# Kernel optimization log

Measured on AMD Instinct MI355X. Metric: run time of the kernel, lower is better.

Reference implementation:

```python
import jax, jax.numpy as jnp
import numpy as np

B, H_IMG, W_IMG, C_IMG, NP = 8, 384, 384, 3, 6
DELTA = 10
TOL = 1e-3
LAM = 0.05          # lambda_ (Charbonnier scale)
MAX_ITER = 12
RIDGE = 1e-6


def _cubic(s):
    # Keys bicubic convolution kernel, a = -0.5
    a = -0.5
    s = jnp.abs(s)
    s2 = s * s
    s3 = s2 * s
    w1 = (a + 2.0) * s3 - (a + 3.0) * s2 + 1.0
    w2 = a * s3 - 5.0 * a * s2 + 8.0 * a * s - 4.0 * a
    return jnp.where(s <= 1.0, w1, jnp.where(s < 2.0, w2, 0.0))


def _bicubic(I, xg, yg):
    # I: [b,H,W,C]; xg,yg: [b,H,W] sample coordinates
    Bn, Hh, Ww, C = I.shape
    x0 = jnp.floor(xg)
    y0 = jnp.floor(yg)
    tx = xg - x0
    ty = yg - y0
    xi = x0.astype(jnp.int32)
    yi = y0.astype(jnp.int32)
    bidx = jnp.arange(Bn)[:, None, None]
    out = jnp.zeros(I.shape, I.dtype)
    for j in range(4):           # fixed 4x4 tap stencil
        wy = _cubic(ty - (j - 1))
        yy = jnp.clip(yi + (j - 1), 0, Hh - 1)
        for k in range(4):
            wx = _cubic(tx - (k - 1))
            xx = jnp.clip(xi + (k - 1), 0, Ww - 1)
            out = out + (wy * wx)[..., None] * I[bidx, yy, xx, :]
    return out


def _params2matrix(p):
    # AFFINITY: x' = x + p0 + p2*x + p3*y ; y' = y + p1 + p4*x + p5*y
    zero = jnp.zeros_like(p[:, 0])
    one = jnp.ones_like(p[:, 0])
    r0 = jnp.stack([1.0 + p[:, 2], p[:, 3], p[:, 0]], -1)
    r1 = jnp.stack([p[:, 4], 1.0 + p[:, 5], p[:, 1]], -1)
    r2 = jnp.stack([zero, zero, one], -1)
    return jnp.stack([r0, r1, r2], 1)


def _matrix2params(M):
    M = M / M[:, 2:3, 2:3]
    return jnp.stack([M[:, 0, 2], M[:, 1, 2], M[:, 0, 0] - 1.0,
                      M[:, 0, 1], M[:, 1, 0], M[:, 1, 1] - 1.0], -1)


def _gradients(I):
    # central differences, zero-padded at the borders (as in compute_gradients)
    Ix = jnp.pad((I[:, :, 2:, :] - I[:, :, :-2, :]) * 0.5,
                 ((0, 0), (0, 0), (1, 1), (0, 0)))
    Iy = jnp.pad((I[:, 2:, :, :] - I[:, :-2, :, :]) * 0.5,
                 ((0, 0), (1, 1), (0, 0), (0, 0)))
    return Ix, Iy


def setup_inputs() -> dict:
    key = jax.random.key(0)
    k1, k2 = jax.random.split(key)
    I1 = jax.random.uniform(k1, (B, H_IMG, W_IMG, C_IMG), jnp.float32)
    I2 = jax.random.uniform(k2, (B, H_IMG, W_IMG, C_IMG), jnp.float32)
    p = jnp.zeros((B, NP), jnp.float32)
    return {"I1": I1, "I2": I2, "p": p}


def _forward(I1, I2, p):
    Bn, Hh, Ww, C = I1.shape
    x = jnp.arange(Ww, dtype=jnp.float32)
    y = jnp.arange(Hh, dtype=jnp.float32)
    X, Y = jnp.meshgrid(x, y)
    ones = jnp.ones_like(X)
    zeros = jnp.zeros_like(X)
    # AFFINITY Jacobian, split into Jx / Jy halves: [H,W,6]
    Jx = jnp.stack([ones, zeros, X, Y, zeros, zeros], -1)
    Jy = jnp.stack([zeros, ones, zeros, zeros, X, Y], -1)
    Ix, Iy = _gradients(I1)
    # steepest-descent images: [b,H,W,C,6]
    DIJ = Ix[..., None] * Jx[None, :, :, None, :] + Iy[..., None] * Jy[None, :, :, None, :]
    rows_ok = (jnp.arange(Hh) >= DELTA) & (jnp.arange(Hh) < Hh - DELTA)
    cols_ok = (jnp.arange(Ww) >= DELTA) & (jnp.arange(Ww) < Ww - DELTA)
    valid1 = (rows_ok[:, None] & cols_ok[None, :])[None, :, :, None]  # [1,H,W,1]
    coords = jnp.stack([X, Y, ones], 0)  # [3,H,W]
    eye = jnp.eye(NP, dtype=jnp.float32)

    def warp(pcur):
        M = _params2matrix(pcur)
        g = jnp.einsum('bij,jhw->bihw', M, coords)
        xg, yg = g[:, 0], g[:, 1]
        Iw = _bicubic(I2, xg, yg)
        gx = jnp.round(xg).astype(jnp.int32)
        gy = jnp.round(yg).astype(jnp.int32)
        wmask = ((gx >= DELTA) & (gx <= Ww - DELTA) &
                 (gy >= DELTA) & (gy <= Hh - DELTA))[..., None]
        return Iw, wmask

    def step(carry, _):
        pcur, done = carry
        Iw, wmask = carry_warp = warp(pcur)
        m = wmask & valid1
        DI = jnp.where(m, Iw - I1, 0.0)
        # Charbonnier influence weight psi(e) = 1/sqrt(1 + (e/lam)^2)
        w = jnp.where(m, jax.lax.rsqrt(1.0 + (DI / LAM) ** 2), 0.0)
        bvec = jnp.einsum('bhwcm,bhwc->bm', DIJ, w * DI)
        Hm = jnp.einsum('bhwcm,bhwcn->bmn', DIJ * w[..., None], DIJ)
        dp = jnp.linalg.solve(Hm + RIDGE * eye, bvec[..., None])[..., 0]
        # inverse-compositional update: W(p) <- W(p) o W(dp)^-1
        Mn = _params2matrix(pcur) @ jnp.linalg.inv(_params2matrix(dp))
        p_new = _matrix2params(Mn)
        conv = jnp.linalg.norm(dp, axis=-1) < TOL
        p_out = jnp.where(done[:, None], pcur, p_new)
        return (p_out, done | conv), None

    (pf, _), _ = jax.lax.scan(step, (p, jnp.zeros((Bn,), bool)), None, length=MAX_ITER)
    Iw, wmask = warp(pf)
    m = wmask & valid1
    DI = jnp.where(m, Iw - I1, 0.0)
    rho = 2.0 * LAM * LAM * (jnp.sqrt(1.0 + (DI / LAM) ** 2) - 1.0)
    mb = jnp.broadcast_to(m, DI.shape)
    cnt = jnp.sum(mb.astype(jnp.float32), axis=(1, 2, 3))
    err = jnp.sum(jnp.where(mb, rho, 0.0), axis=(1, 2, 3)) / jnp.maximum(cnt, 1.0)
    return pf, err, DI, Iw


def reference(I1, I2, p):
    return _forward(I1, I2, p)
```

## Files before the change

kernel.cpp:

```cpp
#include <hip/hip_runtime.h>
#include <math.h>

#define BB 8
#define HH 384
#define WW 384
#define NPAR 6
#define DEL 10
#define MAXIT 12
#define NACC 24
#define HWPIX (HH*WW)
#define NRT4 91
#define NR2 8
#define W_STG 76
#define PITCH2 77
#define NWIN 6
#define NR2F 6
#define PITCHF 141
#define WSF 140
#define KB_ 8
#define SPS 32

typedef float vf4 __attribute__((ext_vector_type(4)));
typedef vf4 uvf4 __attribute__((aligned(4)));
typedef float f2v __attribute__((ext_vector_type(2), aligned(4)));
typedef float lf4 __attribute__((ext_vector_type(4)));

__device__ __forceinline__ vf4 ldv4(const float* p) { return *(const uvf4*)p; }

__device__ __forceinline__ lf4 ldpx3(const float* __restrict__ Ib, int pixoff) {
    const int fo = pixoff * 3;
    if (fo + 4 <= HWPIX * 3) {
        vf4 v = ldv4(Ib + fo);
        return (lf4){v.x, v.y, v.z, 0.f};
    }
    vf4 v = ldv4(Ib + fo - 1);
    return (lf4){v.y, v.z, v.w, 0.f};
}

__device__ __forceinline__ float cubicw(float s) {
    s = fabsf(s);
    float s2 = s * s, s3 = s2 * s;
    float w1 = 1.5f * s3 - 2.5f * s2 + 1.0f;
    float w2 = -0.5f * s3 + 2.5f * s2 - 4.0f * s + 2.0f;
    return (s <= 1.0f) ? w1 : ((s < 2.0f) ? w2 : 0.0f);
}

__device__ __forceinline__ void bicubic3_fast(const float* __restrict__ Ib, double xg, double yg, float Iw[3]) {
    double fx = floor(xg), fy = floor(yg);
    float tx = (float)(xg - fx), ty = (float)(yg - fy);
    int xi = (int)fx, yi = (int)fy;
    float wx[4], wyv[4];
#pragma unroll
    for (int k = 0; k < 4; k++) { wx[k] = cubicw(tx - (float)(k - 1)); wyv[k] = cubicw(ty - (float)(k - 1)); }
    Iw[0] = 0.f; Iw[1] = 0.f; Iw[2] = 0.f;
    const float* base = Ib + (yi - 1) * (WW * 3) + (xi - 1) * 3;
#pragma unroll
    for (int j = 0; j < 4; j++) {
        const float* r = base + j * (WW * 3);
        vf4 v0 = ldv4(r), v1 = ldv4(r + 4), v2 = ldv4(r + 8);
        float r0 = fmaf(wx[0], v0.x, 0.f); r0 = fmaf(wx[1], v0.w, r0); r0 = fmaf(wx[2], v1.z, r0); r0 = fmaf(wx[3], v2.y, r0);
        float r1 = fmaf(wx[0], v0.y, 0.f); r1 = fmaf(wx[1], v1.x, r1); r1 = fmaf(wx[2], v1.w, r1); r1 = fmaf(wx[3], v2.z, r1);
        float r2 = fmaf(wx[0], v0.z, 0.f); r2 = fmaf(wx[1], v1.y, r2); r2 = fmaf(wx[2], v2.x, r2); r2 = fmaf(wx[3], v2.w, r2);
        Iw[0] = fmaf(wyv[j], r0, Iw[0]);
        Iw[1] = fmaf(wyv[j], r1, Iw[1]);
        Iw[2] = fmaf(wyv[j], r2, Iw[2]);
    }
}

__device__ __forceinline__ void bicubic3_gen(const float* __restrict__ Ib, double xg, double yg, float Iw[3]) {
    double fx = floor(xg), fy = floor(yg);
    int xi = (int)fx, yi = (int)fy;
    float tx = (float)(xg - fx), ty = (float)(yg - fy);
    float wx[4], wyv[4];
    int xx[4], yy[4];
#pragma unroll
    for (int k = 0; k < 4; k++) {
        wx[k] = cubicw(tx - (float)(k - 1)); wyv[k] = cubicw(ty - (float)(k - 1));
        xx[k] = min(max(xi + k - 1, 0), WW - 1);
        yy[k] = min(max(yi + k - 1, 0), HH - 1);
    }
    Iw[0] = 0.f; Iw[1] = 0.f; Iw[2] = 0.f;
#pragma unroll
    for (int j = 0; j < 4; j++) {
        const float* row = Ib + yy[j] * (WW * 3);
        float r0 = 0.f, r1 = 0.f, r2 = 0.f;
#pragma unroll
        for (int k = 0; k < 4; k++) {
            const float* q = row + xx[k] * 3;
            r0 = fmaf(wx[k], q[0], r0); r1 = fmaf(wx[k], q[1], r1); r2 = fmaf(wx[k], q[2], r2);
        }
        Iw[0] = fmaf(wyv[j], r0, Iw[0]);
        Iw[1] = fmaf(wyv[j], r1, Iw[1]);
        Iw[2] = fmaf(wyv[j], r2, Iw[2]);
    }
}

template<int P>
__device__ __forceinline__ void bicubic3_lds(const lf4* __restrict__ T, int ssx, int ssy,
                                             float tx, float ty, float Iw[3]) {
    float wx[4], wyv[4];
#pragma unroll
    for (int k = 0; k < 4; k++) { wx[k] = cubicw(tx - (float)(k - 1)); wyv[k] = cubicw(ty - (float)(k - 1)); }
    Iw[0] = 0.f; Iw[1] = 0.f; Iw[2] = 0.f;
    const lf4* bp = T + (ssy - 1) * P + (ssx - 1);
#pragma unroll
    for (int j = 0; j < 4; j++) {
        lf4 t0 = bp[j * P + 0], t1 = bp[j * P + 1], t2 = bp[j * P + 2], t3 = bp[j * P + 3];
        float r0 = fmaf(wx[0], t0.x, 0.f); r0 = fmaf(wx[1], t1.x, r0); r0 = fmaf(wx[2], t2.x, r0); r0 = fmaf(wx[3], t3.x, r0);
        float r1 = fmaf(wx[0], t0.y, 0.f); r1 = fmaf(wx[1], t1.y, r1); r1 = fmaf(wx[2], t2.y, r1); r1 = fmaf(wx[3], t3.y, r1);
        float r2 = fmaf(wx[0], t0.z, 0.f); r2 = fmaf(wx[1], t1.z, r2); r2 = fmaf(wx[2], t2.z, r2); r2 = fmaf(wx[3], t3.z, r2);
        Iw[0] = fmaf(wyv[j], r0, Iw[0]);
        Iw[1] = fmaf(wyv[j], r1, Iw[1]);
        Iw[2] = fmaf(wyv[j], r2, Iw[2]);
    }
}

__device__ __forceinline__
void solve6_fast(const double* __restrict__ Sb, const double* __restrict__ pc,
                 double pn[6], int* convp) {
    const double b0 = Sb[0], b1 = Sb[3], b2 = Sb[1], b3 = Sb[2], b4 = Sb[4], b5 = Sb[5];
    const double h00 = Sb[6]  + 1e-6, h01 = Sb[12], h02 = Sb[7],  h03 = Sb[8],  h04 = Sb[13], h05 = Sb[14];
    const double h11 = Sb[18] + 1e-6, h12 = Sb[13], h13 = Sb[14], h14 = Sb[19], h15 = Sb[20];
    const double h22 = Sb[9]  + 1e-6, h23 = Sb[10], h24 = Sb[15], h25 = Sb[16];
    const double h33 = Sb[11] + 1e-6, h34 = Sb[16], h35 = Sb[17];
    const double h44 = Sb[21] + 1e-6, h45 = Sb[22];
    const double h55 = Sb[23] + 1e-6;

    const double l00 = sqrt(h00);
    const double i0 = 1.0 / l00;
    const double l10 = h01 * i0, l20 = h02 * i0, l30 = h03 * i0, l40 = h04 * i0, l50 = h05 * i0;
    const double l11 = sqrt(h11 - l10 * l10);
    const double i1 = 1.0 / l11;
    const double l21 = (h12 - l20 * l10) * i1;
    const double l31 = (h13 - l30 * l10) * i1;
    const double l41 = (h14 - l40 * l10) * i1;
    const double l51 = (h15 - l50 * l10) * i1;
    const double l22 = sqrt(h22 - l20 * l20 - l21 * l21);
    const double i2 = 1.0 / l22;
    const double l32 = (h23 - l30 * l20 - l31 * l21) * i2;
    const double l42 = (h24 - l40 * l20 - l41 * l21) * i2;
    const double l52 = (h25 - l50 * l20 - l51 * l21) * i2;
    const double l33 = sqrt(h33 - l30 * l30 - l31 * l31 - l32 * l32);
    const double i3 = 1.0 / l33;
    const double l43 = (h34 - l40 * l30 - l41 * l31 - l42 * l32) * i3;
    const double l53 = (h35 - l50 * l30 - l51 * l31 - l52 * l32) * i3;
    const double l44 = sqrt(h44 - l40 * l40 - l41 * l41 - l42 * l42 - l43 * l43);
    const double i4 = 1.0 / l44;
    const double l54 = (h45 - l50 * l40 - l51 * l41 - l52 * l42 - l53 * l43) * i4;
    const double l55 = sqrt(h55 - l50 * l50 - l51 * l51 - l52 * l52 - l53 * l53 - l54 * l54);
    const double i5 = 1.0 / l55;

    const double y0 = b0 * i0;
    const double y1 = (b1 - l10 * y0) * i1;
    const double y2 = (b2 - l20 * y0 - l21 * y1) * i2;
    const double y3 = (b3 - l30 * y0 - l31 * y1 - l32 * y2) * i3;
    const double y4 = (b4 - l40 * y0 - l41 * y1 - l42 * y2 - l43 * y3) * i4;
    const double y5 = (b5 - l50 * y0 - l51 * y1 - l52 * y2 - l53 * y3 - l54 * y4) * i5;

    const double d5 = y5 * i5;
    const double d4 = (y4 - l54 * d5) * i4;
    const double d3 = (y3 - l43 * d4 - l53 * d5) * i3;
    const double d2 = (y2 - l32 * d3 - l42 * d4 - l52 * d5) * i2;
    const double d1 = (y1 - l21 * d2 - l31 * d3 - l41 * d4 - l51 * d5) * i1;
    const double d0 = (y0 - l10 * d1 - l20 * d2 - l30 * d3 - l40 * d4 - l50 * d5) * i0;

    const double nrm = sqrt(d0*d0 + d1*d1 + d2*d2 + d3*d3 + d4*d4 + d5*d5);
    *convp = (nrm < 1e-3) ? 1 : 0;

    const double m00 = 1.0 + pc[2], m01 = pc[3], m02 = pc[0];
    const double m10 = pc[4], m11 = 1.0 + pc[5], m12 = pc[1];
    const double q00 = 1.0 + d2, q01 = d3, q02 = d0;
    const double q10 = d4, q11 = 1.0 + d5, q12 = d1;
    const double det = q00 * q11 - q01 * q10;
    const double j00 = q11 / det, j01 = -q01 / det;
    const double j10 = -q10 / det, j11 = q00 / det;
    const double jt0 = -(j00 * q02 + j01 * q12);
    const double jt1 = -(j10 * q02 + j11 * q12);
    const double n00 = m00 * j00 + m01 * j10;
    const double n01 = m00 * j01 + m01 * j11;
    const double n02 = m00 * jt0 + m01 * jt1 + m02;
    const double n10 = m10 * j00 + m11 * j10;
    const double n11 = m10 * j01 + m11 * j11;
    const double n12 = m10 * jt0 + m11 * jt1 + m12;
    pn[0] = n02;
    pn[1] = n12;
    pn[2] = n00 - 1.0;
    pn[3] = n01;
    pn[4] = n10;
    pn[5] = n11 - 1.0;
}

extern "C" __global__ __launch_bounds__(256)
void k_init(const float* __restrict__ p0, double* __restrict__ p_store,
            int* __restrict__ done0, double* __restrict__ S_part_all,
            double* __restrict__ Sf_part) {
    const int idx = blockIdx.x * 256 + threadIdx.x;
    const int n = MAXIT * KB_ * BB * SPS;
    for (int i = idx; i < n; i += gridDim.x * 256) S_part_all[i] = 0.0;
    if (blockIdx.x == 0) {
        const int tid = threadIdx.x;
        if (tid < KB_ * BB * 4) Sf_part[tid] = 0.0;
        if (tid < BB * NPAR) p_store[tid] = (double)p0[tid];
        if (tid < BB) done0[tid] = 0;
    }
}

extern "C" __global__ __launch_bounds__(256, 8)
void k_iter(const float* __restrict__ I1, const float* __restrict__ I2,
            const double* __restrict__ p_in, const int* __restrict__ done_in,
            const double* __restrict__ S_in, double* __restrict__ S_out,
            double* __restrict__ p_out_g, int* __restrict__ done_out_g,
            int first) {
    __shared__ __align__(16) double SMEMD[1664];
    __shared__ double Ssum[NACC];
    __shared__ double pbc[NPAR];
    __shared__ int dbc;
    lf4* SMEM = (lf4*)SMEMD;
    const int tid = threadIdx.x;
    const int b = blockIdx.y;
    const int tix = blockIdx.x;
    const int rt = tix / NWIN, win = tix - rt * NWIN;
    const int y0 = 10 + rt * 4;
    const int x0 = 10 + win * 64;
    const int sx0 = x0 - 6;

    double pp[NPAR];
#pragma unroll
    for (int i = 0; i < NPAR; i++) pp[i] = p_in[b * NPAR + i];
    {
        const double pM10 = pp[4], pM11 = 1.0 + pp[5], pM12 = pp[1];
        const double ygc = pM10 * (double)(x0 + 32) + pM11 * ((double)y0 + 1.5) + pM12;
        const int r0 = (int)fmin(fmax(floor(ygc) - 3.0, -100000.0), 100000.0);
        const float* I2b = I2 + (size_t)b * HWPIX * 3;
        for (int i = tid; i < NR2 * W_STG; i += 256) {
            const int r = i / W_STG, c = i - r * W_STG;
            const int gr = min(max(r0 + r, 0), HH - 1);
            const int gc = min(sx0 + c, WW - 1);
            SMEM[r * PITCH2 + c] = ldpx3(I2b, gr * WW + gc);
        }
    }
    const double pM10_ = pp[4], pM11_ = 1.0 + pp[5], pM12_ = pp[1];
    const double ygc_ = pM10_ * (double)(x0 + 32) + pM11_ * ((double)y0 + 1.5) + pM12_;
    const int r0 = (int)fmin(fmax(floor(ygc_) - 3.0, -100000.0), 100000.0);

    if (!first && tid < NACC) {
        double a0 = 0.0, a1 = 0.0;
#pragma unroll
        for (int k = 0; k < KB_; k += 2) {
            a0 += S_in[((size_t)(k * BB + b)) * SPS + tid];
            a1 += S_in[((size_t)((k + 1) * BB + b)) * SPS + tid];
        }
        Ssum[tid] = a0 + a1;
    }
    __syncthreads();

    if (tid == 0) {
        if (first) {
#pragma unroll
            for (int i = 0; i < NPAR; i++) pbc[i] = pp[i];
            dbc = done_in[b];
        } else {
            if (done_in[b]) {
#pragma unroll
                for (int i = 0; i < NPAR; i++) pbc[i] = pp[i];
                dbc = 1;
            } else {
                double pn[6]; int conv;
                solve6_fast(Ssum, p_in + b * NPAR, pn, &conv);
#pragma unroll
                for (int i = 0; i < NPAR; i++) pbc[i] = pn[i];
                dbc = conv;
            }
            if (blockIdx.x == 0) {
#pragma unroll
                for (int i = 0; i < NPAR; i++) p_out_g[b * NPAR + i] = pbc[i];
                done_out_g[b] = dbc;
            }
        }
    }
    __syncthreads();
    if (dbc) return;

    const double M00 = 1.0 + pbc[2], M01 = pbc[3], M02 = pbc[0];
    const double M10 = pbc[4], M11 = 1.0 + pbc[5], M12 = pbc[1];
    const float* I1b = I1 + (size_t)b * HWPIX * 3;
    const float* I2b = I2 + (size_t)b * HWPIX * 3;

    const int wid = tid >> 6, lane = tid & 63;
    const int y = y0 + wid;
    const double Y = (double)y;
    const double Bx = M01 * Y + M02;
    const double By = M11 * Y + M12;

    const int x = x0 + lane;
    const double X = (double)x;
    const double xg = fma(M00, X, Bx);
    const double yg = fma(M10, X, By);
    const double gx = rint(xg), gy = rint(yg);
    const bool ok = (x < WW - DEL) &&
                    (gx >= (double)DEL && gx <= (double)(WW - DEL) &&
                     gy >= (double)DEL && gy <= (double)(HH - DEL));
    const double fx = floor(xg), fy = floor(yg);
    const int xi = (int)fx, yi = (int)fy;
    const float tx = (float)(xg - fx), ty = (float)(yg - fy);
    const int sxi = xi - sx0, syi = yi - r0;
    const bool inwin = ok && (sxi >= 1) && (sxi <= W_STG - 3) && (syi >= 1) && (syi <= NR2 - 3);

    float Iw[3];
    if (ok && !inwin) {
        bicubic3_fast(I2b, xg, yg, Iw);
    } else {
        const int ssx = inwin ? sxi : 8;
        const int ssy = inwin ? syi : 2;
        bicubic3_lds<PITCH2>(SMEM, ssx, ssy, tx, ty, Iw);
    }

    const int xc = min(x, WW - DEL - 1);
    const int pixL = y * WW + xc;
    const float* c = I1b + pixL * 3;
    vf4 u0 = ldv4(c - 3);
    vf4 u1 = ldv4(c + 1);
    float cr2 = c[5];
    vf4 uu = ldv4(c - WW * 3);
    vf4 ud = ldv4(c + WW * 3);

    const float cl[3] = {u0.x, u0.y, u0.z};
    const float cv[3] = {u0.w, u1.x, u1.y};
    const float cr[3] = {u1.z, u1.w, cr2};
    const float cu[3] = {uu.x, uu.y, uu.z};
    const float cd[3] = {ud.x, ud.y, ud.z};

    const float msk = ok ? 1.0f : 0.0f;
    float Af = 0.f, Bf = 0.f, Cf = 0.f, T0f = 0.f, T1f = 0.f;
#pragma unroll
    for (int ch = 0; ch < 3; ch++) {
        const float Ix = (cr[ch] - cl[ch]) * 0.5f;
        const float Iy = (cd[ch] - cu[ch]) * 0.5f;
        const float d = Iw[ch] - cv[ch];
        const float u = d * 20.0f;
        const float w = msk / sqrtf(fmaf(u, u, 1.0f));
        const float wd = w * d;
        T0f = fmaf(Ix, wd, T0f);
        T1f = fmaf(Iy, wd, T1f);
        const float wIx = w * Ix;
        Af = fmaf(wIx, Ix, Af);
        Bf = fmaf(wIx, Iy, Bf);
        Cf = fmaf(w * Iy, Iy, Cf);
    }
    const double T0 = (double)T0f, T1 = (double)T1f;
    const double A = (double)Af, Bd = (double)Bf, Cd = (double)Cf;
    const double XX = X * X;
    double s[13];
    s[0] = T0;  s[1] = T0 * X;
    s[2] = T1;  s[3] = T1 * X;
    s[4] = A;   s[5] = A * X;   s[6] = A * XX;
    s[7] = Bd;  s[8] = Bd * X;  s[9] = Bd * XX;
    s[10] = Cd; s[11] = Cd * X; s[12] = Cd * XX;

#pragma unroll
    for (int i = 0; i < 13; i++) s[i] += __shfl_down(s[i], 32, 64);

    __syncthreads();
    double* scr = SMEMD;
    if (lane < 32) {
        double* o = scr + ((size_t)(wid * 32 + lane)) * 13;
#pragma unroll
        for (int i = 0; i < 13; i++) o[i] = s[i];
    }
    __syncthreads();

    if (tid < NACC) {
        const unsigned long long CLO = 0x9787456454232010ULL;
        const unsigned long long CHI = 0x00000000abcaba78ULL;
        const unsigned long long YPW = 0x0000910910910410ULL;
        const int cix = (int)(((tid < 16) ? (CLO >> (tid * 4)) : (CHI >> ((tid - 16) * 4))) & 0xF);
        const int pw  = (int)((YPW >> (tid * 2)) & 0x3);
        double acc = 0.0;
        for (int w = 0; w < 4; w++) {
            const double* basep = scr + ((size_t)(w * 32)) * 13 + cix;
            double part = 0.0;
            for (int l = 0; l < 32; l++) part += basep[(size_t)l * 13];
            const double Yw = (double)(y0 + w);
            const double f = (pw == 0) ? 1.0 : ((pw == 1) ? Yw : Yw * Yw);
            acc = fma(f, part, acc);
        }
        const int bkt = blockIdx.x & (KB_ - 1);
        unsafeAtomicAdd(&S_out[((size_t)(bkt * BB + b)) * SPS + tid], acc);
    }
}

extern "C" __global__ __launch_bounds__(256, 8)
void k_final_map(const float* __restrict__ I1, const float* __restrict__ I2,
                 const double* __restrict__ p_in, const int* __restrict__ done_in,
                 const double* __restrict__ S_in, double* __restrict__ pf_g,
                 float* __restrict__ DI_out, float* __restrict__ Iw_out,
                 double* __restrict__ Sf_part) {
    __shared__ lf4 I2S[NR2F * PITCHF];
    __shared__ double wsum[4][2];
    __shared__ double Ssum[NACC];
    __shared__ double pbc[NPAR];
    const int tid = threadIdx.x;
    const int b = blockIdx.y;
    const int tix = blockIdx.x;
    const int rt = tix / 3, win = tix - rt * 3;
    const int y0 = rt * 2;
    const int x0 = win * 128;
    const int sx0 = x0 - 6;

    double pp[NPAR];
#pragma unroll
    for (int i = 0; i < NPAR; i++) pp[i] = p_in[b * NPAR + i];
    const double pM10 = pp[4], pM11 = 1.0 + pp[5], pM12 = pp[1];
    const double ygc = pM10 * (double)(x0 + 64) + pM11 * ((double)y0 + 0.5) + pM12;
    const int r0 = (int)fmin(fmax(floor(ygc) - 2.0, -100000.0), 100000.0);
    {
        const float* I2b = I2 + (size_t)b * HWPIX * 3;
        for (int i = tid; i < NR2F * WSF; i += 256) {
            const int r = i / WSF, c = i - r * WSF;
            const int gr = min(max(r0 + r, 0), HH - 1);
            const int gc = min(max(sx0 + c, 0), WW - 1);
            I2S[r * PITCHF + c] = ldpx3(I2b, gr * WW + gc);
        }
    }
    if (tid < NACC) {
        double a0 = 0.0, a1 = 0.0;
#pragma unroll
        for (int k = 0; k < KB_; k += 2) {
            a0 += S_in[((size_t)(k * BB + b)) * SPS + tid];
            a1 += S_in[((size_t)((k + 1) * BB + b)) * SPS + tid];
        }
        Ssum[tid] = a0 + a1;
    }
    __syncthreads();
    if (tid == 0) {
        if (done_in[b]) {
#pragma unroll
            for (int i = 0; i < NPAR; i++) pbc[i] = pp[i];
        } else {
            double pn[6]; int conv;
            solve6_fast(Ssum, p_in + b * NPAR, pn, &conv);
#pragma unroll
            for (int i = 0; i < NPAR; i++) pbc[i] = pn[i];
        }
        if (blockIdx.x == 0) {
#pragma unroll
            for (int i = 0; i < NPAR; i++) pf_g[b * NPAR + i] = pbc[i];
        }
    }
    __syncthreads();

    const double M00 = 1.0 + pbc[2], M01 = pbc[3], M02 = pbc[0];
    const double M10 = pbc[4], M11 = 1.0 + pbc[5], M12 = pbc[1];
    const float* I1b = I1 + (size_t)b * HWPIX * 3;
    const float* I2b = I2 + (size_t)b * HWPIX * 3;
    float* DIb = DI_out + (size_t)b * HWPIX * 3;
    float* Iwb = Iw_out + (size_t)b * HWPIX * 3;

    const int row = tid >> 7;
    const int x = x0 + (tid & 127);
    const int y = y0 + row;
    const int pix = y * WW + x;

    const double X = (double)x, Yd = (double)y;
    const double xg = fma(M00, X, fma(M01, Yd, M02));
    const double yg = fma(M10, X, fma(M11, Yd, M12));
    const double fx = floor(xg), fy = floor(yg);
    const int xi = (int)fx, yi = (int)fy;
    const float tx = (float)(xg - fx), ty = (float)(yg - fy);
    const int sxi = xi - sx0, syi = yi - r0;
    const bool inwin = (sxi >= 1) && (sxi <= WSF - 3) && (syi >= 1) && (syi <= NR2F - 3);

    float Iwp[3];
    if (inwin) bicubic3_lds<PITCHF>(I2S, sxi, syi, tx, ty, Iwp);
    else       bicubic3_gen(I2b, xg, yg, Iwp);

    const bool v1 = (x >= DEL) && (x < WW - DEL) && (y >= DEL) && (y < HH - DEL);
    const double gx = rint(xg), gy = rint(yg);
    const bool wm = (gx >= (double)DEL && gx <= (double)(WW - DEL) &&
                     gy >= (double)DEL && gy <= (double)(HH - DEL));
    const bool mp = v1 && wm;

    const float* cbase = I1b + (size_t)pix * 3;
    const float cv0 = cbase[0], cv1 = cbase[1], cv2 = cbase[2];

    {
        float* wp = Iwb + (size_t)pix * 3;
        *(f2v*)wp = (f2v){Iwp[0], Iwp[1]};
        wp[2] = Iwp[2];
    }
    double rho_s = 0.0, cnt_s = 0.0;
    {
        const float cvv[3] = {cv0, cv1, cv2};
        float dv[3];
#pragma unroll
        for (int ch = 0; ch < 3; ch++) {
            const float d1 = mp ? (Iwp[ch] - cvv[ch]) : 0.0f;
            dv[ch] = d1;
            if (mp) {
                const float u = d1 * 20.0f;
                rho_s += (double)(0.005f * (sqrtf(fmaf(u, u, 1.0f)) - 1.0f));
            }
        }
        if (mp) cnt_s += 3.0;
        float* dp_ = DIb + (size_t)pix * 3;
        *(f2v*)dp_ = (f2v){dv[0], dv[1]};
        dp_[2] = dv[2];
    }

#pragma unroll
    for (int off = 32; off >= 1; off >>= 1) {
        rho_s += __shfl_down(rho_s, off, 64);
        cnt_s += __shfl_down(cnt_s, off, 64);
    }
    const int wv = tid >> 6, lane = tid & 63;
    if (lane == 0) { wsum[wv][0] = rho_s; wsum[wv][1] = cnt_s; }
    __syncthreads();
    if (tid < 2) {
        double sv = wsum[0][tid] + wsum[1][tid] + wsum[2][tid] + wsum[3][tid];
        const int bkt = blockIdx.x & (KB_ - 1);
        unsafeAtomicAdd(&Sf_part[((size_t)(bkt * BB + b)) * 4 + tid], sv);
    }
}

extern "C" __global__ void k_finish(const double* __restrict__ p_fin,
                                    const double* __restrict__ Sf_part,
                                    float* __restrict__ out) {
    const int tid = threadIdx.x;
    if (tid < BB * NPAR) out[tid] = (float)p_fin[tid];
    if (tid >= 48 && tid < 48 + BB) {
        const int b = tid - 48;
        double rs = 0.0, cs = 0.0;
#pragma unroll
        for (int k = 0; k < KB_; k++) {
            rs += Sf_part[((size_t)(k * BB + b)) * 4 + 0];
            cs += Sf_part[((size_t)(k * BB + b)) * 4 + 1];
        }
        out[48 + b] = (float)(rs / fmax(cs, 1.0));
    }
}

extern "C" void kernel_launch(void* const* d_in, const int* in_sizes, int n_in,
                              void* d_out, int out_size, void* d_ws, size_t ws_size,
                              hipStream_t stream) {
    const float* I1 = (const float*)d_in[0];
    const float* I2 = (const float*)d_in[1];
    const float* p0 = (const float*)d_in[2];
    float* out = (float*)d_out;

    double* p_store = (double*)d_ws;
    int* done_flags = (int*)((char*)d_ws + 4992);
    double* S_part_all = (double*)((char*)d_ws + 5408);
    double* Sf_part = (double*)((char*)d_ws + 202016);

    k_init<<<32, 256, 0, stream>>>(p0, p_store, done_flags, S_part_all, Sf_part);

    const size_t SIT = (size_t)KB_ * BB * SPS;
    dim3 gridI(NRT4 * NWIN, BB), blkI(256);
    for (int it = 0; it < MAXIT; it++) {
        const int first = (it == 0) ? 1 : 0;
        const double* p_in = p_store + (size_t)(first ? 0 : (it - 1)) * BB * NPAR;
        const int* d_in_f = done_flags + (first ? 0 : (it - 1)) * BB;
        const double* S_in = S_part_all + (size_t)(first ? 0 : (it - 1)) * SIT;
        k_iter<<<gridI, blkI, 0, stream>>>(I1, I2, p_in, d_in_f, S_in,
                                           S_part_all + (size_t)it * SIT,
                                           p_store + (size_t)it * BB * NPAR,
                                           done_flags + it * BB, first);
    }
    float* DI_out = out + 56;
    float* Iw_out = out + 56 + (size_t)BB * HWPIX * 3;
    dim3 gridF(192 * 3, BB), blkF(256);
    k_final_map<<<gridF, blkF, 0, stream>>>(I1, I2,
                                            p_store + (size_t)11 * BB * NPAR,
                                            done_flags + 11 * BB,
                                            S_part_all + (size_t)11 * SIT,
                                            p_store + (size_t)MAXIT * BB * NPAR,
                                            DI_out, Iw_out, Sf_part);
    k_finish<<<1, 64, 0, stream>>>(p_store + (size_t)MAXIT * BB * NPAR, Sf_part, out);
}
```

Before: 450.2 us.

## Solve 6x6 system once in last-block epilogue instead of per block

Each iteration kernel now uses a two-level atomic counter to detect the last finishing block. Only that block reduces the partial sums and solves the 6x6 system for all batches, writing the next parameters and done flags. Before, every block of the following launch re-read the partials and ran solve6 redundantly in a single thread before starting work. This takes the serial solve off the critical path of all blocks, at the cost of atomic counters, acquire-release ordering and a tail epilogue in one block. It also depends on the release/acquire semantics making the atomically added partials visible to that last block.

```diff
diff --git a/kernel.cpp b/kernel.cpp
--- a/kernel.cpp
+++ b/kernel.cpp
@@ -14,6 +14,9 @@
 #define W_STG 76
 #define PITCH2 77
 #define NWIN 6
+#define NBX (NRT4*NWIN)
+#define L1N 91
+#define L1CNT (6*BB)
 #define NR2F 6
 #define PITCHF 141
 #define WSF 140
@@ -193,10 +196,11 @@
 extern "C" __global__ __launch_bounds__(256)
 void k_init(const float* __restrict__ p0, double* __restrict__ p_store,
             int* __restrict__ done0, double* __restrict__ S_part_all,
-            double* __restrict__ Sf_part) {
+            double* __restrict__ Sf_part, unsigned int* __restrict__ cnt) {
     const int idx = blockIdx.x * 256 + threadIdx.x;
     const int n = MAXIT * KB_ * BB * SPS;
     for (int i = idx; i < n; i += gridDim.x * 256) S_part_all[i] = 0.0;
+    for (int i = idx; i < MAXIT * (L1N + 1); i += gridDim.x * 256) cnt[i] = 0u;
     if (blockIdx.x == 0) {
         const int tid = threadIdx.x;
         if (tid < KB_ * BB * 4) Sf_part[tid] = 0.0;
@@ -208,197 +212,194 @@
 extern "C" __global__ __launch_bounds__(256, 8)
 void k_iter(const float* __restrict__ I1, const float* __restrict__ I2,
             const double* __restrict__ p_in, const int* __restrict__ done_in,
-            const double* __restrict__ S_in, double* __restrict__ S_out,
-            double* __restrict__ p_out_g, int* __restrict__ done_out_g,
-            int first) {
+            double* __restrict__ S_out, double* __restrict__ p_out,
+            int* __restrict__ done_out, unsigned int* __restrict__ c1,
+            unsigned int* __restrict__ c2) {
     __shared__ __align__(16) double SMEMD[1664];
-    __shared__ double Ssum[NACC];
-    __shared__ double pbc[NPAR];
-    __shared__ int dbc;
+    __shared__ int lastflag;
     lf4* SMEM = (lf4*)SMEMD;
+    double* scr = SMEMD;
     const int tid = threadIdx.x;
     const int b = blockIdx.y;
     const int tix = blockIdx.x;
-    const int rt = tix / NWIN, win = tix - rt * NWIN;
-    const int y0 = 10 + rt * 4;
-    const int x0 = 10 + win * 64;
-    const int sx0 = x0 - 6;
-
-    double pp[NPAR];
-#pragma unroll
-    for (int i = 0; i < NPAR; i++) pp[i] = p_in[b * NPAR + i];
-    {
-        const double pM10 = pp[4], pM11 = 1.0 + pp[5], pM12 = pp[1];
-        const double ygc = pM10 * (double)(x0 + 32) + pM11 * ((double)y0 + 1.5) + pM12;
+    const int dn = done_in[b];
+
+    if (!dn) {
+        const int rt = tix / NWIN, win = tix - rt * NWIN;
+        const int y0 = 10 + rt * 4;
+        const int x0 = 10 + win * 64;
+        const int sx0 = x0 - 6;
+
+        double pp[NPAR];
+#pragma unroll
+        for (int i = 0; i < NPAR; i++) pp[i] = p_in[b * NPAR + i];
+        const double M00 = 1.0 + pp[2], M01 = pp[3], M02 = pp[0];
+        const double M10 = pp[4], M11 = 1.0 + pp[5], M12 = pp[1];
+        const float* I1b = I1 + (size_t)b * HWPIX * 3;
+        const float* I2b = I2 + (size_t)b * HWPIX * 3;
+
+        const double ygc = M10 * (double)(x0 + 32) + M11 * ((double)y0 + 1.5) + M12;
         const int r0 = (int)fmin(fmax(floor(ygc) - 3.0, -100000.0), 100000.0);
-        const float* I2b = I2 + (size_t)b * HWPIX * 3;
         for (int i = tid; i < NR2 * W_STG; i += 256) {
             const int r = i / W_STG, c = i - r * W_STG;
             const int gr = min(max(r0 + r, 0), HH - 1);
             const int gc = min(sx0 + c, WW - 1);
             SMEM[r * PITCH2 + c] = ldpx3(I2b, gr * WW + gc);
         }
-    }
-    const double pM10_ = pp[4], pM11_ = 1.0 + pp[5], pM12_ = pp[1];
-    const double ygc_ = pM10_ * (double)(x0 + 32) + pM11_ * ((double)y0 + 1.5) + pM12_;
-    const int r0 = (int)fmin(fmax(floor(ygc_) - 3.0, -100000.0), 100000.0);
-
-    if (!first && tid < NACC) {
-        double a0 = 0.0, a1 = 0.0;
-#pragma unroll
-        for (int k = 0; k < KB_; k += 2) {
-            a0 += S_in[((size_t)(k * BB + b)) * SPS + tid];
-            a1 += S_in[((size_t)((k + 1) * BB + b)) * SPS + tid];
-        }
-        Ssum[tid] = a0 + a1;
-    }
+        __syncthreads();
+
+        const int wid = tid >> 6, lane = tid & 63;
+        const int y = y0 + wid;
+        const double Y = (double)y;
+        const double Bx = M01 * Y + M02;
+        const double By = M11 * Y + M12;
+        const int x = x0 + lane;
+        const double X = (double)x;
+        const double xg = fma(M00, X, Bx);
+        const double yg = fma(M10, X, By);
+        const double gx = rint(xg), gy = rint(yg);
+        const bool ok = (x < WW - DEL) &&
+                        (gx >= (double)DEL && gx <= (double)(WW - DEL) &&
+                         gy >= (double)DEL && gy <= (double)(HH - DEL));
+        const double fx = floor(xg), fy = floor(yg);
+        const int xi = (int)fx, yi = (int)fy;
+        const float tx = (float)(xg - fx), ty = (float)(yg - fy);
+        const int sxi = xi - sx0, syi = yi - r0;
+        const bool inwin = ok && (sxi >= 1) && (sxi <= W_STG - 3) && (syi >= 1) && (syi <= NR2 - 3);
+
+        float Iw[3];
+        if (ok && !inwin) {
+            bicubic3_fast(I2b, xg, yg, Iw);
+        } else {
+            const int ssx = inwin ? sxi : 8;
+            const int ssy = inwin ? syi : 2;
+            bicubic3_lds<PITCH2>(SMEM, ssx, ssy, tx, ty, Iw);
+        }
+
+        const int xc = min(x, WW - DEL - 1);
+        const int pixL = y * WW + xc;
+        const float* c = I1b + pixL * 3;
+        vf4 u0 = ldv4(c - 3);
+        vf4 u1 = ldv4(c + 1);
+        float cr2 = c[5];
+        vf4 uu = ldv4(c - WW * 3);
+        vf4 ud = ldv4(c + WW * 3);
+
+        const float cl[3] = {u0.x, u0.y, u0.z};
+        const float cv[3] = {u0.w, u1.x, u1.y};
+        const float cr[3] = {u1.z, u1.w, cr2};
+        const float cu[3] = {uu.x, uu.y, uu.z};
+        const float cd[3] = {ud.x, ud.y, ud.z};
+
+        const float msk = ok ? 1.0f : 0.0f;
+        float Af = 0.f, Bf = 0.f, Cf = 0.f, T0f = 0.f, T1f = 0.f;
+#pragma unroll
+        for (int ch = 0; ch < 3; ch++) {
+            const float Ix = (cr[ch] - cl[ch]) * 0.5f;
+            const float Iy = (cd[ch] - cu[ch]) * 0.5f;
+            const float d = Iw[ch] - cv[ch];
+            const float u = d * 20.0f;
+            const float w = msk / sqrtf(fmaf(u, u, 1.0f));
+            const float wd = w * d;
+            T0f = fmaf(Ix, wd, T0f);
+            T1f = fmaf(Iy, wd, T1f);
+            const float wIx = w * Ix;
+            Af = fmaf(wIx, Ix, Af);
+            Bf = fmaf(wIx, Iy, Bf);
+            Cf = fmaf(w * Iy, Iy, Cf);
+        }
+        const double T0 = (double)T0f, T1 = (double)T1f;
+        const double A = (double)Af, Bd = (double)Bf, Cd = (double)Cf;
+        const double XX = X * X;
+        double s[13];
+        s[0] = T0;  s[1] = T0 * X;
+        s[2] = T1;  s[3] = T1 * X;
+        s[4] = A;   s[5] = A * X;   s[6] = A * XX;
+        s[7] = Bd;  s[8] = Bd * X;  s[9] = Bd * XX;
+        s[10] = Cd; s[11] = Cd * X; s[12] = Cd * XX;
+
+#pragma unroll
+        for (int i = 0; i < 13; i++) s[i] += __shfl_down(s[i], 32, 64);
+
+        __syncthreads();
+        if (lane < 32) {
+            double* o = scr + ((size_t)(wid * 32 + lane)) * 13;
+#pragma unroll
+            for (int i = 0; i < 13; i++) o[i] = s[i];
+        }
+        __syncthreads();
+
+        if (tid < NACC) {
+            const unsigned long long CLO = 0x9787456454232010ULL;
+            const unsigned long long CHI = 0x00000000abcaba78ULL;
+            const unsigned long long YPW = 0x0000910910910410ULL;
+            const int cix = (int)(((tid < 16) ? (CLO >> (tid * 4)) : (CHI >> ((tid - 16) * 4))) & 0xF);
+            const int pw  = (int)((YPW >> (tid * 2)) & 0x3);
+            double acc = 0.0;
+            for (int w = 0; w < 4; w++) {
+                const double* basep = scr + ((size_t)(w * 32)) * 13 + cix;
+                double part = 0.0;
+                for (int l = 0; l < 32; l++) part += basep[(size_t)l * 13];
+                const double Yw = (double)(y0 + w);
+                const double f = (pw == 0) ? 1.0 : ((pw == 1) ? Yw : Yw * Yw);
+                acc = fma(f, part, acc);
+            }
+            const int bkt = tix & (KB_ - 1);
+            unsafeAtomicAdd(&S_out[((size_t)(bkt * BB + b)) * SPS + tid], acc);
+        }
+    }
+
     __syncthreads();
-
     if (tid == 0) {
-        if (first) {
-#pragma unroll
-            for (int i = 0; i < NPAR; i++) pbc[i] = pp[i];
-            dbc = done_in[b];
-        } else {
-            if (done_in[b]) {
-#pragma unroll
-                for (int i = 0; i < NPAR; i++) pbc[i] = pp[i];
-                dbc = 1;
+        lastflag = 0;
+        const unsigned o1 = __hip_atomic_fetch_add(&c1[tix % L1N], 1u,
+                                __ATOMIC_ACQ_REL, __HIP_MEMORY_SCOPE_AGENT);
+        if (o1 == (unsigned)(L1CNT - 1)) {
+            const unsigned o2 = __hip_atomic_fetch_add(c2, 1u,
+                                    __ATOMIC_ACQ_REL, __HIP_MEMORY_SCOPE_AGENT);
+            if (o2 == (unsigned)(L1N - 1)) lastflag = 1;
+        }
+    }
+    __syncthreads();
+    if (lastflag) {
+        double* FSUM = SMEMD;
+        if (tid < BB * NACC) {
+            const int bt = tid / NACC, a = tid - bt * NACC;
+            double sv = 0.0;
+#pragma unroll
+            for (int k = 0; k < KB_; k++)
+                sv += __hip_atomic_load(&S_out[((size_t)(k * BB + bt)) * SPS + a],
+                                        __ATOMIC_RELAXED, __HIP_MEMORY_SCOPE_AGENT);
+            FSUM[bt * NACC + a] = sv;
+        }
+        __syncthreads();
+        if (tid < BB) {
+            const int bt = tid;
+            double pc[NPAR], pn[NPAR];
+#pragma unroll
+            for (int i = 0; i < NPAR; i++) pc[i] = p_in[bt * NPAR + i];
+            if (done_in[bt]) {
+#pragma unroll
+                for (int i = 0; i < NPAR; i++) p_out[bt * NPAR + i] = pc[i];
+                done_out[bt] = 1;
             } else {
-                double pn[6]; int conv;
-                solve6_fast(Ssum, p_in + b * NPAR, pn, &conv);
-#pragma unroll
-                for (int i = 0; i < NPAR; i++) pbc[i] = pn[i];
-                dbc = conv;
+                int conv;
+                solve6_fast(&FSUM[bt * NACC], pc, pn, &conv);
+#pragma unroll
+                for (int i = 0; i < NPAR; i++) p_out[bt * NPAR + i] = pn[i];
+                done_out[bt] = conv;
             }
-            if (blockIdx.x == 0) {
-#pragma unroll
-                for (int i = 0; i < NPAR; i++) p_out_g[b * NPAR + i] = pbc[i];
-                done_out_g[b] = dbc;
-            }
-        }
-    }
-    __syncthreads();
-    if (dbc) return;
-
-    const double M00 = 1.0 + pbc[2], M01 = pbc[3], M02 = pbc[0];
-    const double M10 = pbc[4], M11 = 1.0 + pbc[5], M12 = pbc[1];
-    const float* I1b = I1 + (size_t)b * HWPIX * 3;
-    const float* I2b = I2 + (size_t)b * HWPIX * 3;
-
-    const int wid = tid >> 6, lane = tid & 63;
-    const int y = y0 + wid;
-    const double Y = (double)y;
-    const double Bx = M01 * Y + M02;
-    const double By = M11 * Y + M12;
-
-    const int x = x0 + lane;
-    const double X = (double)x;
-    const double xg = fma(M00, X, Bx);
-    const double yg = fma(M10, X, By);
-    const double gx = rint(xg), gy = rint(yg);
-    const bool ok = (x < WW - DEL) &&
-                    (gx >= (double)DEL && gx <= (double)(WW - DEL) &&
-                     gy >= (double)DEL && gy <= (double)(HH - DEL));
-    const double fx = floor(xg), fy = floor(yg);
-    const int xi = (int)fx, yi = (int)fy;
-    const float tx = (float)(xg - fx), ty = (float)(yg - fy);
-    const int sxi = xi - sx0, syi = yi - r0;
-    const bool inwin = ok && (sxi >= 1) && (sxi <= W_STG - 3) && (syi >= 1) && (syi <= NR2 - 3);
-
-    float Iw[3];
-    if (ok && !inwin) {
-        bicubic3_fast(I2b, xg, yg, Iw);
-    } else {
-        const int ssx = inwin ? sxi : 8;
-        const int ssy = inwin ? syi : 2;
-        bicubic3_lds<PITCH2>(SMEM, ssx, ssy, tx, ty, Iw);
-    }
-
-    const int xc = min(x, WW - DEL - 1);
-    const int pixL = y * WW + xc;
-    const float* c = I1b + pixL * 3;
-    vf4 u0 = ldv4(c - 3);
-    vf4 u1 = ldv4(c + 1);
-    float cr2 = c[5];
-    vf4 uu = ldv4(c - WW * 3);
-    vf4 ud = ldv4(c + WW * 3);
-
-    const float cl[3] = {u0.x, u0.y, u0.z};
-    const float cv[3] = {u0.w, u1.x, u1.y};
-    const float cr[3] = {u1.z, u1.w, cr2};
-    const float cu[3] = {uu.x, uu.y, uu.z};
-    const float cd[3] = {ud.x, ud.y, ud.z};
-
-    const float msk = ok ? 1.0f : 0.0f;
-    float Af = 0.f, Bf = 0.f, Cf = 0.f, T0f = 0.f, T1f = 0.f;
-#pragma unroll
-    for (int ch = 0; ch < 3; ch++) {
-        const float Ix = (cr[ch] - cl[ch]) * 0.5f;
-        const float Iy = (cd[ch] - cu[ch]) * 0.5f;
-        const float d = Iw[ch] - cv[ch];
-        const float u = d * 20.0f;
-        const float w = msk / sqrtf(fmaf(u, u, 1.0f));
-        const float wd = w * d;
-        T0f = fmaf(Ix, wd, T0f);
-        T1f = fmaf(Iy, wd, T1f);
-        const float wIx = w * Ix;
-        Af = fmaf(wIx, Ix, Af);
-        Bf = fmaf(wIx, Iy, Bf);
-        Cf = fmaf(w * Iy, Iy, Cf);
-    }
-    const double T0 = (double)T0f, T1 = (double)T1f;
-    const double A = (double)Af, Bd = (double)Bf, Cd = (double)Cf;
-    const double XX = X * X;
-    double s[13];
-    s[0] = T0;  s[1] = T0 * X;
-    s[2] = T1;  s[3] = T1 * X;
-    s[4] = A;   s[5] = A * X;   s[6] = A * XX;
-    s[7] = Bd;  s[8] = Bd * X;  s[9] = Bd * XX;
-    s[10] = Cd; s[11] = Cd * X; s[12] = Cd * XX;
-
-#pragma unroll
-    for (int i = 0; i < 13; i++) s[i] += __shfl_down(s[i], 32, 64);
-
-    __syncthreads();
-    double* scr = SMEMD;
-    if (lane < 32) {
-        double* o = scr + ((size_t)(wid * 32 + lane)) * 13;
-#pragma unroll
-        for (int i = 0; i < 13; i++) o[i] = s[i];
-    }
-    __syncthreads();
-
-    if (tid < NACC) {
-        const unsigned long long CLO = 0x9787456454232010ULL;
-        const unsigned long long CHI = 0x00000000abcaba78ULL;
-        const unsigned long long YPW = 0x0000910910910410ULL;
-        const int cix = (int)(((tid < 16) ? (CLO >> (tid * 4)) : (CHI >> ((tid - 16) * 4))) & 0xF);
-        const int pw  = (int)((YPW >> (tid * 2)) & 0x3);
-        double acc = 0.0;
-        for (int w = 0; w < 4; w++) {
-            const double* basep = scr + ((size_t)(w * 32)) * 13 + cix;
-            double part = 0.0;
-            for (int l = 0; l < 32; l++) part += basep[(size_t)l * 13];
-            const double Yw = (double)(y0 + w);
-            const double f = (pw == 0) ? 1.0 : ((pw == 1) ? Yw : Yw * Yw);
-            acc = fma(f, part, acc);
-        }
-        const int bkt = blockIdx.x & (KB_ - 1);
-        unsafeAtomicAdd(&S_out[((size_t)(bkt * BB + b)) * SPS + tid], acc);
+        }
     }
 }
 
 extern "C" __global__ __launch_bounds__(256, 8)
 void k_final_map(const float* __restrict__ I1, const float* __restrict__ I2,
-                 const double* __restrict__ p_in, const int* __restrict__ done_in,
-                 const double* __restrict__ S_in, double* __restrict__ pf_g,
+                 const double* __restrict__ pf_in,
                  float* __restrict__ DI_out, float* __restrict__ Iw_out,
                  double* __restrict__ Sf_part) {
     __shared__ lf4 I2S[NR2F * PITCHF];
     __shared__ double wsum[4][2];
-    __shared__ double Ssum[NACC];
-    __shared__ double pbc[NPAR];
     const int tid = threadIdx.x;
     const int b = blockIdx.y;
     const int tix = blockIdx.x;
@@ -409,52 +410,23 @@
 
     double pp[NPAR];
 #pragma unroll
-    for (int i = 0; i < NPAR; i++) pp[i] = p_in[b * NPAR + i];
-    const double pM10 = pp[4], pM11 = 1.0 + pp[5], pM12 = pp[1];
-    const double ygc = pM10 * (double)(x0 + 64) + pM11 * ((double)y0 + 0.5) + pM12;
-    const int r0 = (int)fmin(fmax(floor(ygc) - 2.0, -100000.0), 100000.0);
-    {
-        const float* I2b = I2 + (size_t)b * HWPIX * 3;
-        for (int i = tid; i < NR2F * WSF; i += 256) {
-            const int r = i / WSF, c = i - r * WSF;
-            const int gr = min(max(r0 + r, 0), HH - 1);
-            const int gc = min(max(sx0 + c, 0), WW - 1);
-            I2S[r * PITCHF + c] = ldpx3(I2b, gr * WW + gc);
-        }
-    }
-    if (tid < NACC) {
-        double a0 = 0.0, a1 = 0.0;
-#pragma unroll
-        for (int k = 0; k < KB_; k += 2) {
-            a0 += S_in[((size_t)(k * BB + b)) * SPS + tid];
-            a1 += S_in[((size_t)((k + 1) * BB + b)) * SPS + tid];
-        }
-        Ssum[tid] = a0 + a1;
-    }
-    __syncthreads();
-    if (tid == 0) {
-        if (done_in[b]) {
-#pragma unroll
-            for (int i = 0; i < NPAR; i++) pbc[i] = pp[i];
-        } else {
-            double pn[6]; int conv;
-            solve6_fast(Ssum, p_in + b * NPAR, pn, &conv);
-#pragma unroll
-            for (int i = 0; i < NPAR; i++) pbc[i] = pn[i];
-        }
-        if (blockIdx.x == 0) {
-#pragma unroll
-            for (int i = 0; i < NPAR; i++) pf_g[b * NPAR + i] = pbc[i];
-        }
-    }
-    __syncthreads();
-
-    const double M00 = 1.0 + pbc[2], M01 = pbc[3], M02 = pbc[0];
-    const double M10 = pbc[4], M11 = 1.0 + pbc[5], M12 = pbc[1];
+    for (int i = 0; i < NPAR; i++) pp[i] = pf_in[b * NPAR + i];
+    const double M00 = 1.0 + pp[2], M01 = pp[3], M02 = pp[0];
+    const double M10 = pp[4], M11 = 1.0 + pp[5], M12 = pp[1];
     const float* I1b = I1 + (size_t)b * HWPIX * 3;
     const float* I2b = I2 + (size_t)b * HWPIX * 3;
     float* DIb = DI_out + (size_t)b * HWPIX * 3;
     float* Iwb = Iw_out + (size_t)b * HWPIX * 3;
+
+    const double ygc = M10 * (double)(x0 + 64) + M11 * ((double)y0 + 0.5) + M12;
+    const int r0 = (int)fmin(fmax(floor(ygc) - 2.0, -100000.0), 100000.0);
+    for (int i = tid; i < NR2F * WSF; i += 256) {
+        const int r = i / WSF, c = i - r * WSF;
+        const int gr = min(max(r0 + r, 0), HH - 1);
+        const int gc = min(max(sx0 + c, 0), WW - 1);
+        I2S[r * PITCHF + c] = ldpx3(I2b, gr * WW + gc);
+    }
+    __syncthreads();
 
     const int row = tid >> 7;
     const int x = x0 + (tid & 127);
@@ -551,28 +523,26 @@
     int* done_flags = (int*)((char*)d_ws + 4992);
     double* S_part_all = (double*)((char*)d_ws + 5408);
     double* Sf_part = (double*)((char*)d_ws + 202016);
-
-    k_init<<<32, 256, 0, stream>>>(p0, p_store, done_flags, S_part_all, Sf_part);
+    unsigned int* cnt = (unsigned int*)((char*)d_ws + 204064);
+
+    k_init<<<32, 256, 0, stream>>>(p0, p_store, done_flags, S_part_all, Sf_part, cnt);
 
     const size_t SIT = (size_t)KB_ * BB * SPS;
-    dim3 gridI(NRT4 * NWIN, BB), blkI(256);
+    dim3 gridI(NBX, BB), blkI(256);
     for (int it = 0; it < MAXIT; it++) {
-        const int first = (it == 0) ? 1 : 0;
-        const double* p_in = p_store + (size_t)(first ? 0 : (it - 1)) * BB * NPAR;
-        const int* d_in_f = done_flags + (first ? 0 : (it - 1)) * BB;
-        const double* S_in = S_part_all + (size_t)(first ? 0 : (it - 1)) * SIT;
-        k_iter<<<gridI, blkI, 0, stream>>>(I1, I2, p_in, d_in_f, S_in,
+        k_iter<<<gridI, blkI, 0, stream>>>(I1, I2,
+                                           p_store + (size_t)it * BB * NPAR,
+                                           done_flags + it * BB,
                                            S_part_all + (size_t)it * SIT,
-                                           p_store + (size_t)it * BB * NPAR,
-                                           done_flags + it * BB, first);
+                                           p_store + (size_t)(it + 1) * BB * NPAR,
+                                           done_flags + (it + 1) * BB,
+                                           cnt + it * (L1N + 1),
+                                           cnt + it * (L1N + 1) + L1N);
     }
     float* DI_out = out + 56;
     float* Iw_out = out + 56 + (size_t)BB * HWPIX * 3;
     dim3 gridF(192 * 3, BB), blkF(256);
     k_final_map<<<gridF, blkF, 0, stream>>>(I1, I2,
-                                            p_store + (size_t)11 * BB * NPAR,
-                                            done_flags + 11 * BB,
-                                            S_part_all + (size_t)11 * SIT,
                                             p_store + (size_t)MAXIT * BB * NPAR,
                                             DI_out, Iw_out, Sf_part);
     k_finish<<<1, 64, 0, stream>>>(p_store + (size_t)MAXIT * BB * NPAR, Sf_part, out);
```

New measurement: 1.526 ms. 239% more time.
